# Optimization experiments

Measured on AMD Instinct MI355X. Metric: run time of the kernel, lower is better.

The kernel has to match this reference:

```python
import jax, jax.numpy as jnp
import numpy as np


def _gru_cell(x, h, Wih, Whh, bih, bhh):
    # PyTorch GRU cell (seq_len=1): gates ordered r, z, n
    gi = x @ Wih.T + bih
    gh = h @ Whh.T + bhh
    i_r, i_z, i_n = jnp.split(gi, 3, axis=-1)
    h_r, h_z, h_n = jnp.split(gh, 3, axis=-1)
    r = jax.nn.sigmoid(i_r + h_r)
    z = jax.nn.sigmoid(i_z + h_z)
    n = jnp.tanh(i_n + r * h_n)
    return (1.0 - z) * n + z * h


def setup_inputs() -> dict:
    key = jax.random.key(0)
    N, K, n_in, H = 4096, 8, 14, 128
    ks = jax.random.split(key, 24)
    s = 0.05
    inp = {
        "towers": jax.random.normal(ks[0], (N, K, n_in), jnp.float32),
        # E_n encoder (Linear -> tanh -> Linear -> tanh)
        "En_W1": jax.random.normal(ks[1], (H, n_in)) * s,
        "En_b1": jnp.zeros((H,)),
        "En_W2": jax.random.normal(ks[2], (H, H)) * s,
        "En_b2": jnp.zeros((H,)),
        # E_e encoder
        "Ee_W1": jax.random.normal(ks[3], (H, 2 * n_in)) * s,
        "Ee_b1": jnp.zeros((H,)),
        "Ee_W2": jax.random.normal(ks[4], (H, H)) * s,
        "Ee_b2": jnp.zeros((H,)),
        # U_gru (node update), input n_in + H
        "U_Wih": jax.random.normal(ks[5], (3 * H, n_in + H)) * s,
        "U_Whh": jax.random.normal(ks[6], (3 * H, H)) * s,
        "U_bih": jnp.zeros((3 * H,)),
        "U_bhh": jnp.zeros((3 * H,)),
        # M_gru (edge update), input 2*(n_in + H)
        "M_Wih": jax.random.normal(ks[7], (3 * H, 2 * (n_in + H))) * s,
        "M_Whh": jax.random.normal(ks[8], (3 * H, H)) * s,
        "M_bih": jnp.zeros((3 * H,)),
        "M_bhh": jnp.zeros((3 * H,)),
        # G_gru (global update), input 2*H
        "G_Wih": jax.random.normal(ks[9], (3 * H, 2 * H)) * s,
        "G_Whh": jax.random.normal(ks[10], (3 * H, H)) * s,
        "G_bih": jnp.zeros((3 * H,)),
        "G_bhh": jnp.zeros((3 * H,)),
        # output head
        "O_W": jax.random.normal(ks[11], (1, H)) * s,
        "O_b": jnp.zeros((1,)),
        "k": 3,
    }
    return inp


def reference(towers, En_W1, En_b1, En_W2, En_b2, Ee_W1, Ee_b1, Ee_W2, Ee_b2,
              U_Wih, U_Whh, U_bih, U_bhh, M_Wih, M_Whh, M_bih, M_bhh,
              G_Wih, G_Whh, G_bih, G_bhh, O_W, O_b, k):
    N, K, n_in = towers.shape
    H = En_W1.shape[0]
    # node state init: h = E_n(towers)
    h = jnp.tanh(jnp.tanh(towers @ En_W1.T + En_b1) @ En_W2.T + En_b2)  # (N,K,H)
    # edge state init: e_h = E_e(all-pairs concat of towers)
    xi = jnp.broadcast_to(towers[:, :, None, :], (N, K, K, n_in))
    xj = jnp.broadcast_to(towers[:, None, :, :], (N, K, K, n_in))
    xx0 = jnp.concatenate([xi, xj], axis=-1)  # (N,K,K,2*n_in)
    e_h = jnp.tanh(jnp.tanh(xx0 @ Ee_W1.T + Ee_b1) @ Ee_W2.T + Ee_b2)  # (N,K,K,H)
    # mask[i,j] = 1 iff j == i+1 (the nested-loop mask is a shifted identity)
    mask = jnp.eye(K, k=1, dtype=towers.dtype)
    e = e_h
    D = n_in + H
    for _ in range(k):
        # edge_fn: all-pairs concat of [towers, h] fed through GRU cell
        xh = jnp.concatenate([towers, h], axis=-1)  # (N,K,D)
        a = jnp.broadcast_to(xh[:, :, None, :], (N, K, K, D))
        b = jnp.broadcast_to(xh[:, None, :, :], (N, K, K, D))
        exx = jnp.concatenate([a, b], axis=-1).reshape(-1, 2 * D)
        e_h = _gru_cell(exx, e_h.reshape(-1, H), M_Wih, M_Whh, M_bih, M_bhh)
        e = e_h.reshape(N, K, K, H)
        # node_fn: masked sum selects e[:, i, i+1]
        edges = jnp.einsum('nijh,ij->nih', e, mask)  # (N,K,H)
        nx = jnp.concatenate([towers, edges], axis=-1).reshape(-1, D)
        h = _gru_cell(nx, h.reshape(-1, H), U_Wih, U_Whh, U_bih, U_bhh).reshape(N, K, H)
        e_h = e_h  # state carried
    # global_fn
    h_sum = h.sum(axis=1)  # (N,H)
    e_sum = jnp.einsum('nijh,ij->nh', e, mask)  # (N,H)
    gx = jnp.concatenate([h_sum, e_sum], axis=-1)  # (N,2H)
    g = _gru_cell(gx, jnp.zeros((N, H), towers.dtype), G_Wih, G_Whh, G_bih, G_bhh)
    out = jax.nn.sigmoid((g @ O_W.T + O_b).reshape(N))
    return out
```

## Files before the change

kernel.cpp:

```cpp
#include <hip/hip_runtime.h>
#include <hip/hip_bf16.h>

typedef __hip_bfloat16 bf16;
typedef unsigned short ush;
typedef short s16x8 __attribute__((ext_vector_type(8)));
typedef ush u16x4 __attribute__((ext_vector_type(4)));
typedef float f32x4 __attribute__((ext_vector_type(4)));

#define DEV __device__ __forceinline__

DEV float rcp_f(float x) { return __builtin_amdgcn_rcpf(x); }
DEV float sigmoid_f(float x) { return rcp_f(1.f + __expf(-x)); }
DEV float tanh_f(float x) { return 1.f - 2.f * rcp_f(__expf(2.f * x) + 1.f); }

DEV float u2f(ush u) { unsigned int v = ((unsigned int)u) << 16; float f; __builtin_memcpy(&f, &v, 4); return f; }
DEV ush f2u(float f) { bf16 h = __float2bfloat16(f); ush u; __builtin_memcpy(&u, &h, 2); return u; }

DEV f32x4 MFMA(s16x8 a, s16x8 b, f32x4 c) {
  return __builtin_amdgcn_mfma_f32_16x16x32_bf16(a, b, c, 0, 0, 0);
}

DEV s16x8 z8() {
  s16x8 v;
  for (int z = 0; z < 8; ++z) v[z] = 0;
  return v;
}

DEV int swz_idx(int row, int kk) { return row * 32 + (((kk >> 3) ^ ((row >> 1) & 3)) << 3) + (kk & 7); }
DEV int swz_blk(int row, int blk) { return row * 32 + ((blk ^ ((row >> 1) & 3)) << 3); }


__global__ __launch_bounds__(256) void prep_all(
    const float* __restrict__ towers,
    const float* __restrict__ MWih, const float* __restrict__ MWhh,
    const float* __restrict__ UWih, const float* __restrict__ UWhh,
    const float* __restrict__ EnW1, const float* __restrict__ EnW2,
    const float* __restrict__ EeW1, const float* __restrict__ EeW2,
    const float* __restrict__ MBih, const float* __restrict__ MBhh,
    const float* __restrict__ UBih, const float* __restrict__ UBhh,
    const float* __restrict__ GWih, const float* __restrict__ GWhh,
    const float* __restrict__ GBih, const float* __restrict__ GBhh,
    ush* __restrict__ xh, ush* __restrict__ WPQ, ush* __restrict__ WTh,
    ush* __restrict__ WTu, ush* __restrict__ WBen1, ush* __restrict__ WBen2,
    ush* __restrict__ WBee1, ush* __restrict__ WBee2,
    float* __restrict__ biasM, float* __restrict__ biasU,
    float* __restrict__ WT_G, float* __restrict__ biasG, ush* __restrict__ bn2rep)
{
  const int b = blockIdx.x, t = threadIdx.x;
  if (b < 2048) {
    const int idx = b * 256 + t;
    const int row = idx >> 4, kk = idx & 15;
    xh[row * 144 + kk] = f2u(kk < 14 ? towers[row * 14 + kk] : 0.f);
  } else if (b < 2528) {
    const int idx = (b - 2048) * 256 + t;
    const int ck = idx / 24576, rem = idx % 24576, n = rem >> 5, kk = rem & 31;
    const int k = ck * 32 + kk;
    const int half = (n >= 384);
    const int m = n - half * 384;
    const int g = m >> 7, c = m & 127;
    const int row = g * 128 + c;
    int col = -1;
    if (k < 14)                  col = k;
    else if (k >= 16 && k < 144) col = k - 2;
    if (half && col >= 0)        col += 142;
    WPQ[idx] = f2u((col >= 0) ? MWih[row * 284 + col] : 0.f);
  } else if (b < 2720) {
    const int idx = (b - 2528) * 256 + t;
    const int ck = idx / 12288, rem = idx % 12288, n = rem >> 5, kk = rem & 31;
    const int g = n >> 7, c = n & 127;
    WTh[idx] = f2u(MWhh[(g * 128 + c) * 128 + ck * 32 + kk]);
  } else if (b < 3296) {
    const int idx = (b - 2720) * 256 + t;
    const int ck = idx >> 14, n = (idx >> 5) & 511, kk = idx & 31;
    const int k = ck * 32 + kk, gate = n >> 7, c = n & 127;
    float w = 0.f;
    const int row = (gate == 0) ? c : (gate == 1) ? 128 + c : 256 + c;
    if (k < 160) {
      int col = -1;
      if (k < 16)        { if (k < 14) col = k; }
      else if (k < 144)  col = 14 + (k - 16);
      if (gate != 3 && col >= 0) w = UWih[row * 142 + col];
    } else {
      if (gate != 2) w = UWhh[row * 128 + (k - 160)];
    }
    WTu[ck * 16384 + swz_idx(n, kk)] = f2u(w);
  } else if (b < 3312) {
    const int idx = (b - 3296) * 256 + t;
    const int n = (idx >> 5) & 127, kk = idx & 31;
    WBen1[idx] = f2u(kk < 14 ? EnW1[n * 14 + kk] : 0.f);
  } else if (b < 3376) {
    const int idx = (b - 3312) * 256 + t;
    const int ck = idx >> 12, n = (idx >> 5) & 127, kk = idx & 31;
    WBen2[idx] = f2u(EnW2[n * 128 + ck * 32 + kk]);
  } else if (b < 3392) {
    const int idx = (b - 3376) * 256 + t;
    const int n = (idx >> 5) & 127, kk = idx & 31;
    int col = (kk < 16) ? (kk < 14 ? kk : -1) : (kk < 30 ? 14 + (kk - 16) : -1);
    WBee1[idx] = f2u(col >= 0 ? EeW1[n * 28 + col] : 0.f);
    (void)n;
  } else if (b < 3456) {
    const int idx = (b - 3392) * 256 + t;
    const int ck = idx >> 12, n = (idx >> 5) & 127, kk = idx & 31;
    WBee2[idx] = f2u(EeW2[n * 128 + ck * 32 + kk]);
  } else if (b < 3458) {
    const int idx = (b - 3456) * 256 + t;
    const int g = idx >> 7, c = idx & 127;
    float v;
    if (g == 0)      v = MBih[c] + MBhh[c];
    else if (g == 1) v = MBih[128 + c] + MBhh[128 + c];
    else if (g == 2) v = MBih[256 + c];
    else             v = MBhh[256 + c];
    biasM[idx] = v;
  } else if (b < 3460) {
    const int idx = (b - 3458) * 256 + t;
    const int g = idx >> 7, c = idx & 127;
    float v;
    if (g == 0)      v = UBih[c] + UBhh[c];
    else if (g == 1) v = UBih[128 + c] + UBhh[128 + c];
    else if (g == 2) v = UBih[256 + c];
    else             v = UBhh[256 + c];
    biasU[idx] = v;
  } else if (b < 4228) {
    const int idx = (b - 3460) * 256 + t;
    const int kc = idx >> 9, cg = (idx >> 2) & 127, gate = idx & 3;
    const int row = (gate == 0) ? cg : (gate == 1) ? cg + 128 : cg + 256;
    float v = 0.f;
    if (kc < 256) { if (gate != 3) v = GWih[row * 256 + kc]; }
    else          { if (gate != 2) v = GWhh[row * 128 + (kc - 256)]; }
    WT_G[idx] = v;
  } else if (b < 4230) {
    const int idx = (b - 4228) * 256 + t;
    const int cg = idx >> 2, gate = idx & 3;
    float v;
    if (gate == 0)      v = GBih[cg] + GBhh[cg];
    else if (gate == 1) v = GBih[cg + 128] + GBhh[cg + 128];
    else if (gate == 2) v = GBih[cg + 256];
    else                v = GBhh[cg + 256];
    biasG[idx] = v;
  } else {
    const int idx = (b - 4230) * 256 + t;
    bn2rep[idx] = f2u(MBhh[256 + (idx >> 3)]);
  }
}

DEV void pq_phase(ush* As5, const ush* __restrict__ WPQ,
                  const float* __restrict__ biasM, ush* __restrict__ PqT,
                  int rowBase, int lane, int w)
{
  const int quad = lane >> 4, l15 = lane & 15;
  for (int half = 0; half < 2; ++half) {
    f32x4 acc[6][4];
    #pragma unroll
    for (int tl = 0; tl < 6; ++tl)
      #pragma unroll
      for (int rt = 0; rt < 4; ++rt) {
        #pragma unroll
        for (int q = 0; q < 4; ++q) acc[tl][rt][q] = 0.f;
      }
    for (int ck = 0; ck < 5; ++ck) {
      s16x8 af[4];
      #pragma unroll
      for (int rt = 0; rt < 4; ++rt)
        af[rt] = *(const s16x8*)&As5[ck * 2048 + swz_blk(rt * 16 + l15, quad)];
      #pragma unroll
      for (int tl = 0; tl < 6; ++tl) {
        const int n = w * 96 + tl * 16 + l15;
        const s16x8 bf = *(const s16x8*)&WPQ[(ck * 768 + half * 384 + n) * 32 + quad * 8];
        #pragma unroll
        for (int rt = 0; rt < 4; ++rt) acc[tl][rt] = MFMA(af[rt], bf, acc[tl][rt]);
      }
    }
    #pragma unroll
    for (int tl = 0; tl < 6; ++tl) {
      const int col = w * 96 + tl * 16 + l15;
      const float bv = half ? 0.f : biasM[col];
      #pragma unroll
      for (int rt = 0; rt < 4; ++rt) {
        const int row0 = rowBase + rt * 16 + quad * 4;
        const int g = row0 >> 3, n0 = row0 & 7;
        u16x4 wv;
        #pragma unroll
        for (int q = 0; q < 4; ++q) wv[q] = f2u(acc[tl][rt][q] + bv);
        *(u16x4*)&PqT[((size_t)g * 768 + half * 384 + col) * 8 + n0] = wv;
      }
    }
  }
}

DEV void pq_stage_towers(ush* As5, const ush* __restrict__ xh, int rowBase, int t)
{
  const int gm = t >> 2, gb = t & 3, grow = rowBase + gm;
  if (gb < 2) {
    const s16x8 v = *(const s16x8*)(xh + grow * 144 + gb * 8);
    *(s16x8*)&As5[swz_blk(gm, gb)] = v;
  } else {
    *(s16x8*)&As5[4 * 2048 + swz_blk(gm, gb)] = z8();
  }
}

__global__ __launch_bounds__(256, 2) void enc_en_pq(
    ush* __restrict__ xh,
    const ush* __restrict__ WB1, const float* __restrict__ b1,
    const ush* __restrict__ WB2, const float* __restrict__ b2,
    const ush* __restrict__ WPQ, const float* __restrict__ biasM,
    ush* __restrict__ PqT)
{
  __shared__ ush smem[10240];
  ush* A1  = smem;
  ush* Z1  = smem + 1024;
  ush* As5 = smem;
  const int t = threadIdx.x, lane = t & 63, w = t >> 6;
  const int rowBase = blockIdx.x * 64;
  const int quad = lane >> 4, l15 = lane & 15;

  {
    const int gm = t >> 2, gb = t & 3, grow = rowBase + gm;
    s16x8 v = z8();
    if (gb < 2) v = *(const s16x8*)(xh + grow * 144 + gb * 8);
    *(s16x8*)&A1[swz_blk(gm, gb)] = v;
  }
  __syncthreads();

  s16x8 af[4];
  #pragma unroll
  for (int rt = 0; rt < 4; ++rt)
    af[rt] = *(const s16x8*)&A1[swz_blk(rt * 16 + l15, quad)];
  f32x4 acc1[4][2];
  #pragma unroll
  for (int rt = 0; rt < 4; ++rt)
    #pragma unroll
    for (int ct = 0; ct < 2; ++ct) {
      #pragma unroll
      for (int q = 0; q < 4; ++q) acc1[rt][ct][q] = 0.f;
    }
  #pragma unroll
  for (int ct = 0; ct < 2; ++ct) {
    const int n = w * 32 + ct * 16 + l15;
    const s16x8 bf = *(const s16x8*)&WB1[n * 32 + quad * 8];
    #pragma unroll
    for (int rt = 0; rt < 4; ++rt) acc1[rt][ct] = MFMA(af[rt], bf, acc1[rt][ct]);
  }
  #pragma unroll
  for (int ct = 0; ct < 2; ++ct) {
    const int col = w * 32 + ct * 16 + l15;
    const int kk = col & 31;
    #pragma unroll
    for (int rt = 0; rt < 4; ++rt) {
      #pragma unroll
      for (int q = 0; q < 4; ++q) {
        const int m = rt * 16 + quad * 4 + q;
        Z1[w * 2048 + swz_idx(m, kk)] = f2u(tanh_f(acc1[rt][ct][q] + b1[col]));
      }
    }
  }
  __syncthreads();

  f32x4 acc2[4][2];
  #pragma unroll
  for (int rt = 0; rt < 4; ++rt)
    #pragma unroll
    for (int ct = 0; ct < 2; ++ct) {
      #pragma unroll
      for (int q = 0; q < 4; ++q) acc2[rt][ct][q] = 0.f;
    }
  for (int ck2 = 0; ck2 < 4; ++ck2) {
    #pragma unroll
    for (int rt = 0; rt < 4; ++rt)
      af[rt] = *(const s16x8*)&Z1[ck2 * 2048 + swz_blk(rt * 16 + l15, quad)];
    #pragma unroll
    for (int ct = 0; ct < 2; ++ct) {
      const int n = w * 32 + ct * 16 + l15;
      const s16x8 bf = *(const s16x8*)&WB2[(ck2 * 128 + n) * 32 + quad * 8];
      #pragma unroll
      for (int rt = 0; rt < 4; ++rt) acc2[rt][ct] = MFMA(af[rt], bf, acc2[rt][ct]);
    }
  }
  __syncthreads();

  #pragma unroll
  for (int ct = 0; ct < 2; ++ct) {
    const int col = w * 32 + ct * 16 + l15;
    const int k = 16 + col, ck = k >> 5, kk = k & 31;
    #pragma unroll
    for (int rt = 0; rt < 4; ++rt) {
      #pragma unroll
      for (int q = 0; q < 4; ++q) {
        const int r = rt * 16 + quad * 4 + q;
        const ush hv = f2u(tanh_f(acc2[rt][ct][q] + b2[col]));
        xh[(rowBase + r) * 144 + 16 + col] = hv;
        As5[ck * 2048 + swz_idx(r, kk)] = hv;
      }
    }
  }
  pq_stage_towers(As5, xh, rowBase, t);
  __syncthreads();
  pq_phase(As5, WPQ, biasM, PqT, rowBase, lane, w);
}

DEV void edge_sparse_gru(ush* As, ush* __restrict__ eh,
                         const ush* __restrict__ WTh,
                         const ush* __restrict__ PqT,
                         const ush* __restrict__ bn2rep,
                         int G0, int t)
{
  const int lane = t & 63, w = t >> 6;
  const int quad = lane >> 4, l15 = lane & 15;

  f32x4 accR[2][4], accZ[2][4], accN1[2][4], accN2[2][4];
  #pragma unroll
  for (int mt = 0; mt < 2; ++mt)
    #pragma unroll
    for (int nt = 0; nt < 4; ++nt) {
      #pragma unroll
      for (int q = 0; q < 4; ++q) { accR[mt][nt][q] = 0.f; accZ[mt][nt][q] = 0.f; accN1[mt][nt][q] = 0.f; accN2[mt][nt][q] = 0.f; }
    }

  #pragma unroll
  for (int ck = 0; ck < 4; ++ck) {
    s16x8 be[4];
    #pragma unroll
    for (int nt = 0; nt < 4; ++nt)
      be[nt] = *(const s16x8*)&As[ck * 2048 + swz_blk(nt * 16 + l15, quad)];
    #pragma unroll
    for (int mt = 0; mt < 2; ++mt) {
      const int nb = w * 32 + mt * 16 + l15;
      const int ko = quad * 8;
      const s16x8 aR = *(const s16x8*)&WTh[(ck * 384 + nb) * 32 + ko];
      const s16x8 aZ = *(const s16x8*)&WTh[(ck * 384 + 128 + nb) * 32 + ko];
      const s16x8 aN = *(const s16x8*)&WTh[(ck * 384 + 256 + nb) * 32 + ko];
      #pragma unroll
      for (int nt = 0; nt < 4; ++nt) {
        accR[mt][nt]  = MFMA(aR, be[nt], accR[mt][nt]);
        accZ[mt][nt]  = MFMA(aZ, be[nt], accZ[mt][nt]);
        accN2[mt][nt] = MFMA(aN, be[nt], accN2[mt][nt]);
      }
    }
  }

  {
    s16x8 bI = z8();
    const int i0 = l15 & 7, hi = l15 >> 3;
    if (quad == hi)                       bI[i0]     = (short)0x3F80;
    else if (quad == 2 + hi && i0 < 7)    bI[i0 + 1] = (short)0x3F80;
    const int part = quad >> 1;
    #pragma unroll
    for (int p = 0; p < 4; ++p) {
      const ush* base = PqT + ((size_t)(G0 + 2 * p + (quad & 1)) * 768 + part * 384) * 8;
      #pragma unroll
      for (int mt = 0; mt < 2; ++mt) {
        const int c = w * 32 + mt * 16 + l15;
        const s16x8 aR  = *(const s16x8*)&base[(c) * 8];
        const s16x8 aZ  = *(const s16x8*)&base[(128 + c) * 8];
        const s16x8 aN1 = *(const s16x8*)&base[(256 + c) * 8];
        s16x8 aN2 = z8();
        if (part == 0) aN2 = *(const s16x8*)&bn2rep[c * 8];
        accR[mt][p]  = MFMA(aR,  bI, accR[mt][p]);
        accZ[mt][p]  = MFMA(aZ,  bI, accZ[mt][p]);
        accN1[mt][p] = MFMA(aN1, bI, accN1[mt][p]);
        accN2[mt][p] = MFMA(aN2, bI, accN2[mt][p]);
      }
    }
  }

  #pragma unroll
  for (int mt = 0; mt < 2; ++mt) {
    const int hc0 = w * 32 + mt * 16 + quad * 4;
    const int ck2 = hc0 >> 5, kkB = hc0 & 31;
    #pragma unroll
    for (int nt = 0; nt < 4; ++nt) {
      const int erow = nt * 16 + l15;
      const int gg = erow >> 3, i = erow & 7;
      if (i == 7) continue;
      const u16x4 hp4 = *(const u16x4*)&As[ck2 * 2048 + swz_blk(erow, kkB >> 3) + (kkB & 7)];
      u16x4 ov;
      #pragma unroll
      for (int q = 0; q < 4; ++q) {
        const float rg = sigmoid_f(accR[mt][nt][q]);
        const float zg = sigmoid_f(accZ[mt][nt][q]);
        const float nn = tanh_f(accN1[mt][nt][q] + rg * accN2[mt][nt][q]);
        const float hp = u2f(hp4[q]);
        ov[q] = f2u(nn + zg * (hp - nn));
      }
      *(u16x4*)&eh[(size_t)((G0 + gg) * 64 + i * 9 + 1) * 128 + hc0] = ov;
    }
  }
}

__global__ __launch_bounds__(256, 2) void edge_first(
    ush* __restrict__ eh, const ush* __restrict__ WTh,
    const ush* __restrict__ PqT, const ush* __restrict__ bn2rep,
    const ush* __restrict__ xh,
    const ush* __restrict__ WB1, const float* __restrict__ b1,
    const ush* __restrict__ WB2, const float* __restrict__ b2)
{
  __shared__ ush smem[17408];
  ush* As = smem;
  ush* A1 = smem + 8192;
  ush* Z1 = smem + 9216;
  const int t = threadIdx.x, lane = t & 63, w = t >> 6;
  const int G0 = blockIdx.x * 8;
  const int quad = lane >> 4, l15 = lane & 15;

  {
    const int gm = t >> 2, gb = t & 3;
    const int gg = gm >> 3, i = gm & 7;
    const int xi = (G0 + gg) * 8 + i;
    const int xj = (i < 7) ? xi + 1 : xi;
    const s16x8 v = (gb < 2) ? *(const s16x8*)(xh + xi * 144 + gb * 8)
                             : *(const s16x8*)(xh + xj * 144 + (gb - 2) * 8);
    *(s16x8*)&A1[swz_blk(gm, gb)] = v;
  }
  __syncthreads();

  s16x8 af[4];
  #pragma unroll
  for (int rt = 0; rt < 4; ++rt)
    af[rt] = *(const s16x8*)&A1[swz_blk(rt * 16 + l15, quad)];
  f32x4 acc1[4][2];
  #pragma unroll
  for (int rt = 0; rt < 4; ++rt)
    #pragma unroll
    for (int ct = 0; ct < 2; ++ct) {
      #pragma unroll
      for (int q = 0; q < 4; ++q) acc1[rt][ct][q] = 0.f;
    }
  #pragma unroll
  for (int ct = 0; ct < 2; ++ct) {
    const int n = w * 32 + ct * 16 + l15;
    const s16x8 bf = *(const s16x8*)&WB1[n * 32 + quad * 8];
    #pragma unroll
    for (int rt = 0; rt < 4; ++rt) acc1[rt][ct] = MFMA(af[rt], bf, acc1[rt][ct]);
  }
  #pragma unroll
  for (int ct = 0; ct < 2; ++ct) {
    const int col = w * 32 + ct * 16 + l15;
    const int kk = col & 31;
    #pragma unroll
    for (int rt = 0; rt < 4; ++rt) {
      #pragma unroll
      for (int q = 0; q < 4; ++q) {
        const int m = rt * 16 + quad * 4 + q;
        Z1[w * 2048 + swz_idx(m, kk)] = f2u(tanh_f(acc1[rt][ct][q] + b1[col]));
      }
    }
  }
  __syncthreads();

  f32x4 acc2[4][2];
  #pragma unroll
  for (int rt = 0; rt < 4; ++rt)
    #pragma unroll
    for (int ct = 0; ct < 2; ++ct) {
      #pragma unroll
      for (int q = 0; q < 4; ++q) acc2[rt][ct][q] = 0.f;
    }
  for (int ck2 = 0; ck2 < 4; ++ck2) {
    #pragma unroll
    for (int rt = 0; rt < 4; ++rt)
      af[rt] = *(const s16x8*)&Z1[ck2 * 2048 + swz_blk(rt * 16 + l15, quad)];
    #pragma unroll
    for (int ct = 0; ct < 2; ++ct) {
      const int n = w * 32 + ct * 16 + l15;
      const s16x8 bf = *(const s16x8*)&WB2[(ck2 * 128 + n) * 32 + quad * 8];
      #pragma unroll
      for (int rt = 0; rt < 4; ++rt) acc2[rt][ct] = MFMA(af[rt], bf, acc2[rt][ct]);
    }
  }
  #pragma unroll
  for (int ct = 0; ct < 2; ++ct) {
    const int col = w * 32 + ct * 16 + l15;
    const int kk = col & 31;
    #pragma unroll
    for (int rt = 0; rt < 4; ++rt) {
      #pragma unroll
      for (int q = 0; q < 4; ++q) {
        const int r = rt * 16 + quad * 4 + q;
        As[(col >> 5) * 2048 + swz_idx(r, kk)] = f2u(tanh_f(acc2[rt][ct][q] + b2[col]));
      }
    }
  }
  __syncthreads();

  edge_sparse_gru(As, eh, WTh, PqT, bn2rep, G0, t);
}

__global__ __launch_bounds__(256, 2) void edge_last(
    ush* __restrict__ eh, const ush* __restrict__ WTh,
    const ush* __restrict__ PqT, const ush* __restrict__ bn2rep)
{
  __shared__ ush As[8192];
  const int t = threadIdx.x;
  const int G0 = blockIdx.x * 8;

  {
    const int gm = t >> 2, gb = t & 3;
    const int gg = gm >> 3, i = gm & 7;
    const ush* src = eh + (size_t)((G0 + gg) * 64 + i * 9 + 1) * 128;
    #pragma unroll
    for (int ck = 0; ck < 4; ++ck) {
      s16x8 v = z8();
      if (i < 7) v = *(const s16x8*)(src + ck * 32 + gb * 8);
      *(s16x8*)&As[ck * 2048 + swz_blk(gm, gb)] = v;
    }
  }
  __syncthreads();

  edge_sparse_gru(As, eh, WTh, PqT, bn2rep, G0, t);
}

template<int PQ>
__global__ __launch_bounds__(256, 2) void gru_node_pq(
    ush* __restrict__ xh, const ush* __restrict__ eh,
    const ush* __restrict__ WT, const float* __restrict__ bias,
    const ush* __restrict__ WPQ, const float* __restrict__ biasM,
    ush* __restrict__ PqT)
{
  constexpr int NCH = 9, XCH = 5;
  __shared__ ush smem[10240];
  ush* As5 = smem;
  const int t = threadIdx.x, lane = t & 63, w = t >> 6;
  const int rowBase = blockIdx.x * 64;
  const int gm = t >> 2, gb = t & 3, grow = rowBase + gm;
  const int l15 = lane & 15, quad = lane >> 4;

  f32x4 accR[4][2], accZ[4][2], accN1[4][2], accN2[4][2];
  #pragma unroll
  for (int rt = 0; rt < 4; ++rt)
    #pragma unroll
    for (int s = 0; s < 2; ++s) {
      #pragma unroll
      for (int q = 0; q < 4; ++q) { accR[rt][s][q] = 0.f; accZ[rt][s][q] = 0.f; accN1[rt][s][q] = 0.f; accN2[rt][s][q] = 0.f; }
    }

  auto stage = [&](int ck) {
    const int k0 = ck * 32 + gb * 8;
    s16x8 v = z8();
    if (k0 < 16)       v = *(const s16x8*)(xh + grow * 144 + k0);
    else if (k0 < 144) {
      const int i = grow & 7;
      if (i < 7) v = *(const s16x8*)(eh + (size_t)(grow * 8 + i + 1) * 128 + (k0 - 16));
    } else if (k0 >= 160) {
      v = *(const s16x8*)(xh + grow * 144 + 16 + (k0 - 160));
    }
    *(s16x8*)&smem[(ck & 1) * 2048 + swz_blk(gm, gb)] = v;
  };

  stage(0);
  __syncthreads();

  for (int ck = 0; ck < NCH; ++ck) {
    if (ck + 1 < NCH) stage(ck + 1);

    const ush* Wc = WT + ck * 16384;
    const ush* Ac = smem + (ck & 1) * 2048;
    s16x8 af[4];
    #pragma unroll
    for (int rt = 0; rt < 4; ++rt)
      af[rt] = *(const s16x8*)&Ac[swz_blk(rt * 16 + l15, quad)];
    if (ck < XCH) {
      #pragma unroll
      for (int s = 0; s < 2; ++s) {
        const int nb = w * 32 + s * 16 + l15;
        const s16x8 bR = *(const s16x8*)&Wc[swz_blk(0 * 128 + nb, quad)];
        const s16x8 bZ = *(const s16x8*)&Wc[swz_blk(1 * 128 + nb, quad)];
        const s16x8 bN = *(const s16x8*)&Wc[swz_blk(2 * 128 + nb, quad)];
        #pragma unroll
        for (int rt = 0; rt < 4; ++rt) {
          accR[rt][s]  = MFMA(af[rt], bR, accR[rt][s]);
          accZ[rt][s]  = MFMA(af[rt], bZ, accZ[rt][s]);
          accN1[rt][s] = MFMA(af[rt], bN, accN1[rt][s]);
        }
      }
    } else {
      #pragma unroll
      for (int s = 0; s < 2; ++s) {
        const int nb = w * 32 + s * 16 + l15;
        const s16x8 bR = *(const s16x8*)&Wc[swz_blk(0 * 128 + nb, quad)];
        const s16x8 bZ = *(const s16x8*)&Wc[swz_blk(1 * 128 + nb, quad)];
        const s16x8 bN = *(const s16x8*)&Wc[swz_blk(3 * 128 + nb, quad)];
        #pragma unroll
        for (int rt = 0; rt < 4; ++rt) {
          accR[rt][s]  = MFMA(af[rt], bR, accR[rt][s]);
          accZ[rt][s]  = MFMA(af[rt], bZ, accZ[rt][s]);
          accN2[rt][s] = MFMA(af[rt], bN, accN2[rt][s]);
        }
      }
    }
    __syncthreads();
  }

  #pragma unroll
  for (int s = 0; s < 2; ++s) {
    const int hcol = w * 32 + s * 16 + l15;
    const float bR = bias[hcol], bZ = bias[128 + hcol], bN1 = bias[256 + hcol], bN2 = bias[384 + hcol];
    const int k = 16 + hcol, ckh = k >> 5, kkh = k & 31;
    #pragma unroll
    for (int rt = 0; rt < 4; ++rt) {
      #pragma unroll
      for (int q = 0; q < 4; ++q) {
        const int r = rt * 16 + quad * 4 + q;
        const int row = rowBase + r;
        const float hp = u2f(xh[row * 144 + 16 + hcol]);
        const float rg = sigmoid_f(accR[rt][s][q] + bR);
        const float zg = sigmoid_f(accZ[rt][s][q] + bZ);
        const float nn = tanh_f(accN1[rt][s][q] + bN1 + rg * (accN2[rt][s][q] + bN2));
        const ush hv = f2u(nn + zg * (hp - nn));
        xh[row * 144 + 16 + hcol] = hv;
        if (PQ) As5[ckh * 2048 + swz_idx(r, kkh)] = hv;
      }
    }
  }
  if (PQ) {
    pq_stage_towers(As5, xh, rowBase, t);
    __syncthreads();
    pq_phase(As5, WPQ, biasM, PqT, rowBase, lane, w);
  }
}

__global__ __launch_bounds__(256) void sums2(const ush* __restrict__ xh, const ush* __restrict__ eh,
                                             float* __restrict__ hsum, float* __restrict__ esum) {
  const int idx = blockIdx.x * 256 + threadIdx.x;
  const int n = idx >> 7, hh = idx & 127;
  float hs = 0.f, es = 0.f;
  #pragma unroll
  for (int i = 0; i < 8; ++i) hs += u2f(xh[(n * 8 + i) * 144 + 16 + hh]);
  #pragma unroll
  for (int i = 0; i < 7; ++i) es += u2f(eh[(size_t)((n * 8 + i) * 8 + i + 1) * 128 + hh]);
  hsum[idx] = hs;
  esum[idx] = es;
}

__global__ __launch_bounds__(256) void gru_global_out(
    const float* __restrict__ hsum, const float* __restrict__ esum,
    const float* __restrict__ WT, const float* __restrict__ bias,
    const float* __restrict__ OW, const float* __restrict__ Ob,
    float* __restrict__ out)
{
  constexpr int KT = 384;
  __shared__ float4 ATl4[KT * 4];
  __shared__ float4 Bl4[16 * 128];
  __shared__ float gmat[16 * 128];
  __shared__ float red[16 * 4];
  float* ATl = (float*)ATl4;
  const int t = threadIdx.x;
  const int rowBase = blockIdx.x * 16;
  for (int idx = t; idx < KT * 16; idx += 256) {
    const int kc = idx >> 4, r = idx & 15, grow = rowBase + r;
    float v = 0.f;
    if (kc < 128)      v = hsum[grow * 128 + kc];
    else if (kc < 256) v = esum[grow * 128 + (kc - 128)];
    ATl[idx] = v;
  }
  const int c = t & 127, rh = t >> 7;
  float accR[8], accZ[8], accN1[8];
  #pragma unroll
  for (int rr = 0; rr < 8; ++rr) { accR[rr] = 0.f; accZ[rr] = 0.f; accN1[rr] = 0.f; }
  const float4* WT4 = (const float4*)WT;
  for (int ck = 0; ck < 16; ++ck) {
    __syncthreads();
    #pragma unroll
    for (int ii = 0; ii < 8; ++ii) { const int idx = t + ii * 256; Bl4[idx] = WT4[ck * 2048 + idx]; }
    __syncthreads();
    const int kb = ck * 16;
    #pragma unroll
    for (int kcl = 0; kcl < 16; ++kcl) {
      const float4 wv = Bl4[kcl * 128 + c];
      const float4 a0 = ATl4[(kb + kcl) * 4 + rh * 2];
      const float4 a1 = ATl4[(kb + kcl) * 4 + rh * 2 + 1];
      const float av[8] = {a0.x, a0.y, a0.z, a0.w, a1.x, a1.y, a1.z, a1.w};
      #pragma unroll
      for (int rr = 0; rr < 8; ++rr) {
        accR[rr]  += wv.x * av[rr];
        accZ[rr]  += wv.y * av[rr];
        accN1[rr] += wv.z * av[rr];
      }
    }
  }
  const float4 bb = ((const float4*)bias)[c];
  const float ow = OW[c];
  #pragma unroll
  for (int rr = 0; rr < 8; ++rr) {
    const float rg = sigmoid_f(accR[rr] + bb.x);
    const float zg = sigmoid_f(accZ[rr] + bb.y);
    const float nn = tanh_f(accN1[rr] + bb.z + rg * bb.w);
    gmat[(rh * 8 + rr) * 128 + c] = (1.f - zg) * nn * ow;
  }
  __syncthreads();
  if (t < 64) {
    const int r = t >> 2, part = t & 3;
    float s = 0.f;
    #pragma unroll
    for (int cc = 0; cc < 32; ++cc) s += gmat[r * 128 + part * 32 + cc];
    red[r * 4 + part] = s;
  }
  __syncthreads();
  if (t < 16) {
    const float s = red[t * 4] + red[t * 4 + 1] + red[t * 4 + 2] + red[t * 4 + 3];
    out[rowBase + t] = sigmoid_f(s + Ob[0]);
  }
}

extern "C" void kernel_launch(void* const* d_in, const int* in_sizes, int n_in,
                              void* d_out, int out_size, void* d_ws, size_t ws_size,
                              hipStream_t stream)
{
  (void)in_sizes; (void)n_in; (void)out_size; (void)ws_size;
  const float* towers = (const float*)d_in[0];
  const float* EnW1 = (const float*)d_in[1];
  const float* EnB1 = (const float*)d_in[2];
  const float* EnW2 = (const float*)d_in[3];
  const float* EnB2 = (const float*)d_in[4];
  const float* EeW1 = (const float*)d_in[5];
  const float* EeB1 = (const float*)d_in[6];
  const float* EeW2 = (const float*)d_in[7];
  const float* EeB2 = (const float*)d_in[8];
  const float* UWih = (const float*)d_in[9];
  const float* UWhh = (const float*)d_in[10];
  const float* UBih = (const float*)d_in[11];
  const float* UBhh = (const float*)d_in[12];
  const float* MWih = (const float*)d_in[13];
  const float* MWhh = (const float*)d_in[14];
  const float* MBih = (const float*)d_in[15];
  const float* MBhh = (const float*)d_in[16];
  const float* GWih = (const float*)d_in[17];
  const float* GWhh = (const float*)d_in[18];
  const float* GBih = (const float*)d_in[19];
  const float* GBhh = (const float*)d_in[20];
  const float* OW   = (const float*)d_in[21];
  const float* Ob   = (const float*)d_in[22];

  char* ws = (char*)d_ws;
  size_t off = 0;
  auto take = [&](size_t b) { void* p = ws + off; off = (off + b + 255) & ~(size_t)255; return p; };
  ush*   xh     = (ush*)take((size_t)32768 * 144 * 2);
  ush*   eh     = (ush*)take((size_t)262144 * 128 * 2);
  ush*   PqT    = (ush*)take((size_t)4096 * 768 * 8 * 2);
  float* hsum   = (float*)take((size_t)4096 * 128 * 4);
  float* esum   = (float*)take((size_t)4096 * 128 * 4);
  ush*   WPQ    = (ush*)take((size_t)5 * 768 * 32 * 2);
  ush*   WTh    = (ush*)take((size_t)4 * 384 * 32 * 2);
  ush*   WTu    = (ush*)take((size_t)9 * 512 * 32 * 2);
  ush*   WBen1  = (ush*)take((size_t)128 * 32 * 2);
  ush*   WBen2  = (ush*)take((size_t)4 * 128 * 32 * 2);
  ush*   WBee1  = (ush*)take((size_t)128 * 32 * 2);
  ush*   WBee2  = (ush*)take((size_t)4 * 128 * 32 * 2);
  float* biasM  = (float*)take(512 * 4);
  float* biasU  = (float*)take(512 * 4);
  float* WT_G   = (float*)take((size_t)384 * 512 * 4);
  float* biasG  = (float*)take(512 * 4);
  ush*   bn2rep = (ush*)take(128 * 8 * 2);

  prep_all<<<4234, 256, 0, stream>>>(
      towers, MWih, MWhh, UWih, UWhh, EnW1, EnW2, EeW1, EeW2,
      MBih, MBhh, UBih, UBhh, GWih, GWhh, GBih, GBhh,
      xh, WPQ, WTh, WTu, WBen1, WBen2, WBee1, WBee2,
      biasM, biasU, WT_G, biasG, bn2rep);

  enc_en_pq<<<512, 256, 0, stream>>>(xh, WBen1, EnB1, WBen2, EnB2, WPQ, biasM, PqT);

  edge_first<<<512, 256, 0, stream>>>(eh, WTh, PqT, bn2rep, xh, WBee1, EeB1, WBee2, EeB2);
  gru_node_pq<1><<<512, 256, 0, stream>>>(xh, eh, WTu, biasU, WPQ, biasM, PqT);
  edge_last<<<512, 256, 0, stream>>>(eh, WTh, PqT, bn2rep);
  gru_node_pq<1><<<512, 256, 0, stream>>>(xh, eh, WTu, biasU, WPQ, biasM, PqT);
  edge_last<<<512, 256, 0, stream>>>(eh, WTh, PqT, bn2rep);
  gru_node_pq<0><<<512, 256, 0, stream>>>(xh, eh, WTu, biasU, WPQ, biasM, PqT);

  sums2<<<2048, 256, 0, stream>>>(xh, eh, hsum, esum);
  gru_global_out<<<256, 256, 0, stream>>>(hsum, esum, WT_G, biasG, OW, Ob, (float*)d_out);
}
```

Measured before the change: 295.4 us.

## Fuse encoder, edge/node GRU iterations and sums into one persistent-LDS megakernel

```diff
diff --git a/kernel.cpp b/kernel.cpp
--- a/kernel.cpp
+++ b/kernel.cpp
@@ -198,19 +198,16 @@
   }
 }
 
-__global__ __launch_bounds__(256, 2) void enc_en_pq(
-    ush* __restrict__ xh,
-    const ush* __restrict__ WB1, const float* __restrict__ b1,
-    const ush* __restrict__ WB2, const float* __restrict__ b2,
-    const ush* __restrict__ WPQ, const float* __restrict__ biasM,
-    ush* __restrict__ PqT)
-{
-  __shared__ ush smem[10240];
-  ush* A1  = smem;
-  ush* Z1  = smem + 1024;
-  ush* As5 = smem;
-  const int t = threadIdx.x, lane = t & 63, w = t >> 6;
-  const int rowBase = blockIdx.x * 64;
+DEV void enc_body(ush* SC, ush* __restrict__ xh,
+                  const ush* __restrict__ WB1, const float* __restrict__ b1,
+                  const ush* __restrict__ WB2, const float* __restrict__ b2,
+                  const ush* __restrict__ WPQ, const float* __restrict__ biasM,
+                  ush* __restrict__ PqT, int rowBase, int t)
+{
+  ush* A1  = SC;
+  ush* Z1  = SC + 1024;
+  ush* As5 = SC;
+  const int lane = t & 63, w = t >> 6;
   const int quad = lane >> 4, l15 = lane & 15;
 
   {
@@ -297,15 +294,105 @@
   pq_phase(As5, WPQ, biasM, PqT, rowBase, lane, w);
 }
 
-DEV void edge_sparse_gru(ush* As, ush* __restrict__ eh,
-                         const ush* __restrict__ WTh,
-                         const ush* __restrict__ PqT,
-                         const ush* __restrict__ bn2rep,
-                         int G0, int t)
-{
+DEV void ee_body(ush* As_e, ush* SC, const ush* __restrict__ xh,
+                 const ush* __restrict__ WB1, const float* __restrict__ b1,
+                 const ush* __restrict__ WB2, const float* __restrict__ b2,
+                 int G0, int t)
+{
+  ush* A1 = SC;
+  ush* Z1 = SC + 1024;
   const int lane = t & 63, w = t >> 6;
   const int quad = lane >> 4, l15 = lane & 15;
 
+  {
+    const int gm = t >> 2, gb = t & 3;
+    const int gg = gm >> 3, i = gm & 7;
+    const int xi = (G0 + gg) * 8 + i;
+    const int xj = (i < 7) ? xi + 1 : xi;
+    const s16x8 v = (gb < 2) ? *(const s16x8*)(xh + xi * 144 + gb * 8)
+                             : *(const s16x8*)(xh + xj * 144 + (gb - 2) * 8);
+    *(s16x8*)&A1[swz_blk(gm, gb)] = v;
+  }
+  __syncthreads();
+
+  s16x8 af[4];
+  #pragma unroll
+  for (int rt = 0; rt < 4; ++rt)
+    af[rt] = *(const s16x8*)&A1[swz_blk(rt * 16 + l15, quad)];
+  f32x4 acc1[4][2];
+  #pragma unroll
+  for (int rt = 0; rt < 4; ++rt)
+    #pragma unroll
+    for (int ct = 0; ct < 2; ++ct) {
+      #pragma unroll
+      for (int q = 0; q < 4; ++q) acc1[rt][ct][q] = 0.f;
+    }
+  #pragma unroll
+  for (int ct = 0; ct < 2; ++ct) {
+    const int n = w * 32 + ct * 16 + l15;
+    const s16x8 bf = *(const s16x8*)&WB1[n * 32 + quad * 8];
+    #pragma unroll
+    for (int rt = 0; rt < 4; ++rt) acc1[rt][ct] = MFMA(af[rt], bf, acc1[rt][ct]);
+  }
+  #pragma unroll
+  for (int ct = 0; ct < 2; ++ct) {
+    const int col = w * 32 + ct * 16 + l15;
+    const int kk = col & 31;
+    #pragma unroll
+    for (int rt = 0; rt < 4; ++rt) {
+      #pragma unroll
+      for (int q = 0; q < 4; ++q) {
+        const int m = rt * 16 + quad * 4 + q;
+        Z1[w * 2048 + swz_idx(m, kk)] = f2u(tanh_f(acc1[rt][ct][q] + b1[col]));
+      }
+    }
+  }
+  __syncthreads();
+
+  f32x4 acc2[4][2];
+  #pragma unroll
+  for (int rt = 0; rt < 4; ++rt)
+    #pragma unroll
+    for (int ct = 0; ct < 2; ++ct) {
+      #pragma unroll
+      for (int q = 0; q < 4; ++q) acc2[rt][ct][q] = 0.f;
+    }
+  for (int ck2 = 0; ck2 < 4; ++ck2) {
+    #pragma unroll
+    for (int rt = 0; rt < 4; ++rt)
+      af[rt] = *(const s16x8*)&Z1[ck2 * 2048 + swz_blk(rt * 16 + l15, quad)];
+    #pragma unroll
+    for (int ct = 0; ct < 2; ++ct) {
+      const int n = w * 32 + ct * 16 + l15;
+      const s16x8 bf = *(const s16x8*)&WB2[(ck2 * 128 + n) * 32 + quad * 8];
+      #pragma unroll
+      for (int rt = 0; rt < 4; ++rt) acc2[rt][ct] = MFMA(af[rt], bf, acc2[rt][ct]);
+    }
+  }
+  #pragma unroll
+  for (int ct = 0; ct < 2; ++ct) {
+    const int col = w * 32 + ct * 16 + l15;
+    const int kk = col & 31;
+    #pragma unroll
+    for (int rt = 0; rt < 4; ++rt) {
+      #pragma unroll
+      for (int q = 0; q < 4; ++q) {
+        const int r = rt * 16 + quad * 4 + q;
+        As_e[(col >> 5) * 2048 + swz_idx(r, kk)] = f2u(tanh_f(acc2[rt][ct][q] + b2[col]));
+      }
+    }
+  }
+}
+
+DEV void edge_gru_lds(ush* As_e,
+                      const ush* __restrict__ WTh,
+                      const ush* __restrict__ PqT,
+                      const ush* __restrict__ bn2rep,
+                      int G0, int t)
+{
+  const int lane = t & 63, w = t >> 6;
+  const int quad = lane >> 4, l15 = lane & 15;
+
   f32x4 accR[2][4], accZ[2][4], accN1[2][4], accN2[2][4];
   #pragma unroll
   for (int mt = 0; mt < 2; ++mt)
@@ -320,7 +407,7 @@
     s16x8 be[4];
     #pragma unroll
     for (int nt = 0; nt < 4; ++nt)
-      be[nt] = *(const s16x8*)&As[ck * 2048 + swz_blk(nt * 16 + l15, quad)];
+      be[nt] = *(const s16x8*)&As_e[ck * 2048 + swz_blk(nt * 16 + l15, quad)];
     #pragma unroll
     for (int mt = 0; mt < 2; ++mt) {
       const int nb = w * 32 + mt * 16 + l15;
@@ -362,6 +449,8 @@
     }
   }
 
+  __syncthreads();
+
   #pragma unroll
   for (int mt = 0; mt < 2; ++mt) {
     const int hc0 = w * 32 + mt * 16 + quad * 4;
@@ -369,9 +458,8 @@
     #pragma unroll
     for (int nt = 0; nt < 4; ++nt) {
       const int erow = nt * 16 + l15;
-      const int gg = erow >> 3, i = erow & 7;
-      if (i == 7) continue;
-      const u16x4 hp4 = *(const u16x4*)&As[ck2 * 2048 + swz_blk(erow, kkB >> 3) + (kkB & 7)];
+      ush* cell = &As_e[ck2 * 2048 + swz_blk(erow, kkB >> 3) + (kkB & 7)];
+      const u16x4 hp4 = *(const u16x4*)cell;
       u16x4 ov;
       #pragma unroll
       for (int q = 0; q < 4; ++q) {
@@ -381,145 +469,20 @@
         const float hp = u2f(hp4[q]);
         ov[q] = f2u(nn + zg * (hp - nn));
       }
-      *(u16x4*)&eh[(size_t)((G0 + gg) * 64 + i * 9 + 1) * 128 + hc0] = ov;
-    }
-  }
-}
-
-__global__ __launch_bounds__(256, 2) void edge_first(
-    ush* __restrict__ eh, const ush* __restrict__ WTh,
-    const ush* __restrict__ PqT, const ush* __restrict__ bn2rep,
-    const ush* __restrict__ xh,
-    const ush* __restrict__ WB1, const float* __restrict__ b1,
-    const ush* __restrict__ WB2, const float* __restrict__ b2)
-{
-  __shared__ ush smem[17408];
-  ush* As = smem;
-  ush* A1 = smem + 8192;
-  ush* Z1 = smem + 9216;
-  const int t = threadIdx.x, lane = t & 63, w = t >> 6;
-  const int G0 = blockIdx.x * 8;
-  const int quad = lane >> 4, l15 = lane & 15;
-
-  {
-    const int gm = t >> 2, gb = t & 3;
-    const int gg = gm >> 3, i = gm & 7;
-    const int xi = (G0 + gg) * 8 + i;
-    const int xj = (i < 7) ? xi + 1 : xi;
-    const s16x8 v = (gb < 2) ? *(const s16x8*)(xh + xi * 144 + gb * 8)
-                             : *(const s16x8*)(xh + xj * 144 + (gb - 2) * 8);
-    *(s16x8*)&A1[swz_blk(gm, gb)] = v;
-  }
-  __syncthreads();
-
-  s16x8 af[4];
-  #pragma unroll
-  for (int rt = 0; rt < 4; ++rt)
-    af[rt] = *(const s16x8*)&A1[swz_blk(rt * 16 + l15, quad)];
-  f32x4 acc1[4][2];
-  #pragma unroll
-  for (int rt = 0; rt < 4; ++rt)
-    #pragma unroll
-    for (int ct = 0; ct < 2; ++ct) {
-      #pragma unroll
-      for (int q = 0; q < 4; ++q) acc1[rt][ct][q] = 0.f;
-    }
-  #pragma unroll
-  for (int ct = 0; ct < 2; ++ct) {
-    const int n = w * 32 + ct * 16 + l15;
-    const s16x8 bf = *(const s16x8*)&WB1[n * 32 + quad * 8];
-    #pragma unroll
-    for (int rt = 0; rt < 4; ++rt) acc1[rt][ct] = MFMA(af[rt], bf, acc1[rt][ct]);
-  }
-  #pragma unroll
-  for (int ct = 0; ct < 2; ++ct) {
-    const int col = w * 32 + ct * 16 + l15;
-    const int kk = col & 31;
-    #pragma unroll
-    for (int rt = 0; rt < 4; ++rt) {
-      #pragma unroll
-      for (int q = 0; q < 4; ++q) {
-        const int m = rt * 16 + quad * 4 + q;
-        Z1[w * 2048 + swz_idx(m, kk)] = f2u(tanh_f(acc1[rt][ct][q] + b1[col]));
-      }
-    }
-  }
-  __syncthreads();
-
-  f32x4 acc2[4][2];
-  #pragma unroll
-  for (int rt = 0; rt < 4; ++rt)
-    #pragma unroll
-    for (int ct = 0; ct < 2; ++ct) {
-      #pragma unroll
-      for (int q = 0; q < 4; ++q) acc2[rt][ct][q] = 0.f;
-    }
-  for (int ck2 = 0; ck2 < 4; ++ck2) {
-    #pragma unroll
-    for (int rt = 0; rt < 4; ++rt)
-      af[rt] = *(const s16x8*)&Z1[ck2 * 2048 + swz_blk(rt * 16 + l15, quad)];
-    #pragma unroll
-    for (int ct = 0; ct < 2; ++ct) {
-      const int n = w * 32 + ct * 16 + l15;
-      const s16x8 bf = *(const s16x8*)&WB2[(ck2 * 128 + n) * 32 + quad * 8];
-      #pragma unroll
-      for (int rt = 0; rt < 4; ++rt) acc2[rt][ct] = MFMA(af[rt], bf, acc2[rt][ct]);
-    }
-  }
-  #pragma unroll
-  for (int ct = 0; ct < 2; ++ct) {
-    const int col = w * 32 + ct * 16 + l15;
-    const int kk = col & 31;
-    #pragma unroll
-    for (int rt = 0; rt < 4; ++rt) {
-      #pragma unroll
-      for (int q = 0; q < 4; ++q) {
-        const int r = rt * 16 + quad * 4 + q;
-        As[(col >> 5) * 2048 + swz_idx(r, kk)] = f2u(tanh_f(acc2[rt][ct][q] + b2[col]));
-      }
-    }
-  }
-  __syncthreads();
-
-  edge_sparse_gru(As, eh, WTh, PqT, bn2rep, G0, t);
-}
-
-__global__ __launch_bounds__(256, 2) void edge_last(
-    ush* __restrict__ eh, const ush* __restrict__ WTh,
-    const ush* __restrict__ PqT, const ush* __restrict__ bn2rep)
-{
-  __shared__ ush As[8192];
-  const int t = threadIdx.x;
-  const int G0 = blockIdx.x * 8;
-
-  {
-    const int gm = t >> 2, gb = t & 3;
-    const int gg = gm >> 3, i = gm & 7;
-    const ush* src = eh + (size_t)((G0 + gg) * 64 + i * 9 + 1) * 128;
-    #pragma unroll
-    for (int ck = 0; ck < 4; ++ck) {
-      s16x8 v = z8();
-      if (i < 7) v = *(const s16x8*)(src + ck * 32 + gb * 8);
-      *(s16x8*)&As[ck * 2048 + swz_blk(gm, gb)] = v;
-    }
-  }
-  __syncthreads();
-
-  edge_sparse_gru(As, eh, WTh, PqT, bn2rep, G0, t);
+      *(u16x4*)cell = ov;
+    }
+  }
 }
 
 template<int PQ>
-__global__ __launch_bounds__(256, 2) void gru_node_pq(
-    ush* __restrict__ xh, const ush* __restrict__ eh,
-    const ush* __restrict__ WT, const float* __restrict__ bias,
-    const ush* __restrict__ WPQ, const float* __restrict__ biasM,
-    ush* __restrict__ PqT)
+DEV void node_body(const ush* As_e, ush* SC, ush* __restrict__ xh,
+                   const ush* __restrict__ WT, const float* __restrict__ bias,
+                   const ush* __restrict__ WPQ, const float* __restrict__ biasM,
+                   ush* __restrict__ PqT, int rowBase, int t)
 {
   constexpr int NCH = 9, XCH = 5;
-  __shared__ ush smem[10240];
-  ush* As5 = smem;
-  const int t = threadIdx.x, lane = t & 63, w = t >> 6;
-  const int rowBase = blockIdx.x * 64;
+  ush* As5 = SC;
+  const int lane = t & 63, w = t >> 6;
   const int gm = t >> 2, gb = t & 3, grow = rowBase + gm;
   const int l15 = lane & 15, quad = lane >> 4;
 
@@ -538,11 +501,14 @@
     if (k0 < 16)       v = *(const s16x8*)(xh + grow * 144 + k0);
     else if (k0 < 144) {
       const int i = grow & 7;
-      if (i < 7) v = *(const s16x8*)(eh + (size_t)(grow * 8 + i + 1) * 128 + (k0 - 16));
+      if (i < 7) {
+        const int ke = k0 - 16;
+        v = *(const s16x8*)&As_e[(ke >> 5) * 2048 + swz_blk(gm, (ke & 31) >> 3)];
+      }
     } else if (k0 >= 160) {
       v = *(const s16x8*)(xh + grow * 144 + 16 + (k0 - 160));
     }
-    *(s16x8*)&smem[(ck & 1) * 2048 + swz_blk(gm, gb)] = v;
+    *(s16x8*)&SC[(ck & 1) * 2048 + swz_blk(gm, gb)] = v;
   };
 
   stage(0);
@@ -552,7 +518,7 @@
     if (ck + 1 < NCH) stage(ck + 1);
 
     const ush* Wc = WT + ck * 16384;
-    const ush* Ac = smem + (ck & 1) * 2048;
+    const ush* Ac = SC + (ck & 1) * 2048;
     s16x8 af[4];
     #pragma unroll
     for (int rt = 0; rt < 4; ++rt)
@@ -617,17 +583,67 @@
   }
 }
 
-__global__ __launch_bounds__(256) void sums2(const ush* __restrict__ xh, const ush* __restrict__ eh,
-                                             float* __restrict__ hsum, float* __restrict__ esum) {
-  const int idx = blockIdx.x * 256 + threadIdx.x;
-  const int n = idx >> 7, hh = idx & 127;
-  float hs = 0.f, es = 0.f;
-  #pragma unroll
-  for (int i = 0; i < 8; ++i) hs += u2f(xh[(n * 8 + i) * 144 + 16 + hh]);
-  #pragma unroll
-  for (int i = 0; i < 7; ++i) es += u2f(eh[(size_t)((n * 8 + i) * 8 + i + 1) * 128 + hh]);
-  hsum[idx] = hs;
-  esum[idx] = es;
+DEV void sums_body(const ush* As_e, const ush* __restrict__ xh,
+                   float* __restrict__ hsum, float* __restrict__ esum,
+                   int G0, int rowBase, int t)
+{
+  #pragma unroll
+  for (int ii = 0; ii < 4; ++ii) {
+    const int p = t + ii * 256;
+    const int gg = p >> 7, hh = p & 127;
+    float es = 0.f;
+    #pragma unroll
+    for (int i = 0; i < 7; ++i) {
+      const int slot = gg * 8 + i;
+      es += u2f(As_e[(hh >> 5) * 2048 + swz_idx(slot, hh & 31)]);
+    }
+    float hs = 0.f;
+    #pragma unroll
+    for (int i = 0; i < 8; ++i)
+      hs += u2f(xh[(rowBase + gg * 8 + i) * 144 + 16 + hh]);
+    hsum[(G0 + gg) * 128 + hh] = hs;
+    esum[(G0 + gg) * 128 + hh] = es;
+  }
+}
+
+__global__ __launch_bounds__(256, 2) void gn_mega(
+    ush* __restrict__ xh,
+    const ush* __restrict__ WBen1, const float* __restrict__ bEn1,
+    const ush* __restrict__ WBen2, const float* __restrict__ bEn2,
+    const ush* __restrict__ WBee1, const float* __restrict__ bEe1,
+    const ush* __restrict__ WBee2, const float* __restrict__ bEe2,
+    const ush* __restrict__ WPQ, const float* __restrict__ biasM,
+    const ush* __restrict__ WTh, const ush* __restrict__ bn2rep,
+    const ush* __restrict__ WTu, const float* __restrict__ biasU,
+    ush* __restrict__ PqT, float* __restrict__ hsum, float* __restrict__ esum)
+{
+  __shared__ ush smem[18432];
+  ush* As_e = smem;
+  ush* SC   = smem + 8192;
+  const int t = threadIdx.x;
+  const int G0 = blockIdx.x * 8, rowBase = blockIdx.x * 64;
+
+  enc_body(SC, xh, WBen1, bEn1, WBen2, bEn2, WPQ, biasM, PqT, rowBase, t);
+  __syncthreads();
+  ee_body(As_e, SC, xh, WBee1, bEe1, WBee2, bEe2, G0, t);
+  __syncthreads();
+
+  edge_gru_lds(As_e, WTh, PqT, bn2rep, G0, t);
+  __syncthreads();
+  node_body<1>(As_e, SC, xh, WTu, biasU, WPQ, biasM, PqT, rowBase, t);
+  __syncthreads();
+
+  edge_gru_lds(As_e, WTh, PqT, bn2rep, G0, t);
+  __syncthreads();
+  node_body<1>(As_e, SC, xh, WTu, biasU, WPQ, biasM, PqT, rowBase, t);
+  __syncthreads();
+
+  edge_gru_lds(As_e, WTh, PqT, bn2rep, G0, t);
+  __syncthreads();
+  node_body<0>(As_e, SC, xh, WTu, biasU, WPQ, biasM, PqT, rowBase, t);
+  __syncthreads();
+
+  sums_body(As_e, xh, hsum, esum, G0, rowBase, t);
 }
 
 __global__ __launch_bounds__(256) void gru_global_out(
@@ -733,7 +749,6 @@
   size_t off = 0;
   auto take = [&](size_t b) { void* p = ws + off; off = (off + b + 255) & ~(size_t)255; return p; };
   ush*   xh     = (ush*)take((size_t)32768 * 144 * 2);
-  ush*   eh     = (ush*)take((size_t)262144 * 128 * 2);
   ush*   PqT    = (ush*)take((size_t)4096 * 768 * 8 * 2);
   float* hsum   = (float*)take((size_t)4096 * 128 * 4);
   float* esum   = (float*)take((size_t)4096 * 128 * 4);
@@ -756,15 +771,9 @@
       xh, WPQ, WTh, WTu, WBen1, WBen2, WBee1, WBee2,
       biasM, biasU, WT_G, biasG, bn2rep);
 
-  enc_en_pq<<<512, 256, 0, stream>>>(xh, WBen1, EnB1, WBen2, EnB2, WPQ, biasM, PqT);
-
-  edge_first<<<512, 256, 0, stream>>>(eh, WTh, PqT, bn2rep, xh, WBee1, EeB1, WBee2, EeB2);
-  gru_node_pq<1><<<512, 256, 0, stream>>>(xh, eh, WTu, biasU, WPQ, biasM, PqT);
-  edge_last<<<512, 256, 0, stream>>>(eh, WTh, PqT, bn2rep);
-  gru_node_pq<1><<<512, 256, 0, stream>>>(xh, eh, WTu, biasU, WPQ, biasM, PqT);
-  edge_last<<<512, 256, 0, stream>>>(eh, WTh, PqT, bn2rep);
-  gru_node_pq<0><<<512, 256, 0, stream>>>(xh, eh, WTu, biasU, WPQ, biasM, PqT);
-
-  sums2<<<2048, 256, 0, stream>>>(xh, eh, hsum, esum);
+  gn_mega<<<512, 256, 0, stream>>>(
+      xh, WBen1, EnB1, WBen2, EnB2, WBee1, EeB1, WBee2, EeB2,
+      WPQ, biasM, WTh, bn2rep, WTu, biasU, PqT, hsum, esum);
+
   gru_global_out<<<256, 256, 0, stream>>>(hsum, esum, WT_G, biasG, OW, Ob, (float*)d_out);
 }
```

After: 369.2 us. 25.0% more time.
